# Kernel tuning notes

Measured on AMD Instinct MI355X. Metric: run time of the kernel, lower is better.

Reference implementation:

```python
import jax, jax.numpy as jnp
import numpy as np

B, S, H = 64, 2048, 512
NEG = -1e9

def setup_inputs() -> dict:
    key = jax.random.key(0)
    k1, k2, k3, k4, k5 = jax.random.split(key, 5)
    encoder_outputs = jax.random.normal(k1, (B, S, H), dtype=jnp.float32)
    mask = jax.random.randint(k2, (B, S), 0, 2).astype(bool)
    W = jax.random.normal(k3, (H, H), dtype=jnp.float32) / np.sqrt(H)
    b = jnp.zeros((H,), dtype=jnp.float32)
    v = jax.random.normal(k4, (H,), dtype=jnp.float32)  # context_vector
    return {"encoder_outputs": encoder_outputs, "mask": mask, "W": W, "b": b, "v": v}

def reference(encoder_outputs, mask, W, b, v):
    # u = tanh(x @ W^T + b): [B,S,H]
    u = jnp.tanh(jnp.einsum('bsh,oh->bso', encoder_outputs, W) + b)
    scores = jnp.einsum('bsh,h->bs', u, v)                 # [B,S]
    scores = jnp.where(mask, scores, NEG)
    attn_weights = jax.nn.softmax(scores, axis=1)          # [B,S]
    weighted_output = jnp.einsum('bsh,bs->bh', encoder_outputs, attn_weights)
    return weighted_output, attn_weights
```

## Files before the change

kernel.cpp:

```cpp
#include <hip/hip_runtime.h>
#include <hip/hip_fp16.h>
#include <stdint.h>

#define NEG_ (-1e9f)

typedef _Float16 f16x8 __attribute__((ext_vector_type(8)));
typedef float    f32x4 __attribute__((ext_vector_type(4)));

__device__ __forceinline__ float fast_tanh(float x) {
  float e = __expf(2.0f * x);
  return (e - 1.0f) * __builtin_amdgcn_rcpf(e + 1.0f);
}

__global__ __launch_bounds__(256) void k0_cvt_w(const float* __restrict__ W,
                                                __half* __restrict__ Wws) {
  int g = blockIdx.x * 256 + threadIdx.x;
  int lane = g & 63;
  int seg  = g >> 6;
  int io = seg & 3, ks = (seg >> 2) & 15, w = seg >> 6;
  int o = w * 64 + io * 16 + (lane & 15);
  int k = ks * 32 + (lane >> 4) * 8;
  const float2* src = (const float2*)(W + (size_t)o * 512 + k);
  __half2 h[4];
#pragma unroll
  for (int j = 0; j < 4; ++j) { float2 f = src[j]; h[j] = __floats2half2_rn(f.x, f.y); }
  uint4 u;
  u.x = *(uint32_t*)&h[0]; u.y = *(uint32_t*)&h[1];
  u.z = *(uint32_t*)&h[2]; u.w = *(uint32_t*)&h[3];
  *(uint4*)(Wws + (size_t)seg * 512 + (size_t)lane * 8) = u;
}

__global__ __launch_bounds__(512, 4) void k1_scores(
    const float* __restrict__ enc, const int* __restrict__ msk,
    const float* __restrict__ bias, const float* __restrict__ ctx,
    const __half* __restrict__ Wws, float* __restrict__ scores,
    float* __restrict__ psum, float* __restrict__ mpart,
    float* __restrict__ lpart) {
  __shared__ __align__(16) __half Xl[64 * 512];
  __shared__ float sred[512];
  __shared__ float pbuf[64];

  const int t = threadIdx.x;
  const int w = t >> 6;
  const int lane = t & 63;
  const int quad = lane >> 4;
  const int l15 = lane & 15;
  const size_t mtile = blockIdx.x;

  f16x8 abuf[3][4];
  auto aload = [&](int slot, int ks) {
    const f16x8* sp = (const f16x8*)(Wws +
        ((size_t)(w * 64 + ks * 4) * 512) + (size_t)lane * 8);
#pragma unroll
    for (int io = 0; io < 4; ++io) abuf[slot][io] = sp[io * 64];
  };

  {
    const float4* Xg = (const float4*)(enc + mtile * (size_t)(64 * 512));
    float4 xr[16];
#pragma unroll
    for (int j = 0; j < 8; ++j) {
      int g = j * 512 + t;
      int s = g >> 6, c = g & 63;
      xr[2 * j]     = Xg[s * 128 + 2 * c];
      xr[2 * j + 1] = Xg[s * 128 + 2 * c + 1];
    }
    aload(0, 0);
    aload(1, 1);
#pragma unroll
    for (int j = 0; j < 8; ++j) {
      int g = j * 512 + t;
      int s = g >> 6, c = g & 63;
      float4 x0 = xr[2 * j];
      float4 x1 = xr[2 * j + 1];
      __half2 h0 = __floats2half2_rn(x0.x, x0.y);
      __half2 h1 = __floats2half2_rn(x0.z, x0.w);
      __half2 h2 = __floats2half2_rn(x1.x, x1.y);
      __half2 h3 = __floats2half2_rn(x1.z, x1.w);
      uint4 u;
      u.x = *(uint32_t*)&h0; u.y = *(uint32_t*)&h1;
      u.z = *(uint32_t*)&h2; u.w = *(uint32_t*)&h3;
      int pc = c ^ (s & 7);
      *(uint4*)&Xl[s * 512 + pc * 8] = u;
    }
  }
  __syncthreads();

  f32x4 acc[4][4];
#pragma unroll
  for (int io = 0; io < 4; ++io)
#pragma unroll
    for (int is = 0; is < 4; ++is) acc[io][is] = (f32x4){0.f, 0.f, 0.f, 0.f};

#pragma unroll
  for (int ks = 0; ks < 16; ++ks) {
    if (ks + 2 < 16) aload((ks + 2) % 3, ks + 2);
    const f16x8* acur = abuf[ks % 3];
#pragma unroll
    for (int is = 0; is < 4; ++is) {
      int s = is * 16 + l15;
      const f16x8 bf = *(const f16x8*)&Xl[s * 512 + (((ks * 4 + quad) ^ (s & 7)) << 3)];
#pragma unroll
      for (int io = 0; io < 4; ++io)
        acc[io][is] = __builtin_amdgcn_mfma_f32_16x16x32_f16(acur[io], bf, acc[io][is], 0, 0, 0);
    }
  }

  float ps[4] = {0.f, 0.f, 0.f, 0.f};
#pragma unroll
  for (int io = 0; io < 4; ++io) {
    int ob = w * 64 + io * 16 + quad * 4;
    float4 b4 = *(const float4*)(bias + ob);
    float4 v4 = *(const float4*)(ctx + ob);
#pragma unroll
    for (int is = 0; is < 4; ++is) {
      const f32x4 a = acc[io][is];
      ps[is] += fast_tanh(a[0] + b4.x) * v4.x + fast_tanh(a[1] + b4.y) * v4.y +
                fast_tanh(a[2] + b4.z) * v4.z + fast_tanh(a[3] + b4.w) * v4.w;
    }
  }
#pragma unroll
  for (int is = 0; is < 4; ++is) {
    ps[is] += __shfl_xor(ps[is], 16, 64);
    ps[is] += __shfl_xor(ps[is], 32, 64);
  }

  __syncthreads();
  if (lane < 16) {
#pragma unroll
    for (int is = 0; is < 4; ++is) sred[w * 64 + is * 16 + lane] = ps[is];
  }
  __syncthreads();
  if (t < 64) {
    float sc = 0.f;
#pragma unroll
    for (int k = 0; k < 8; ++k) sc += sred[k * 64 + t];
    size_t row = mtile * 64 + t;
    float sm = msk[row] ? sc : NEG_;
    scores[row] = sm;
    float m = sm;
#pragma unroll
    for (int off = 32; off >= 1; off >>= 1) m = fmaxf(m, __shfl_xor(m, off, 64));
    float p = __expf(sm - m);
    float l = p;
#pragma unroll
    for (int off = 32; off >= 1; off >>= 1) l += __shfl_xor(l, off, 64);
    pbuf[t] = p;
    if (t == 0) { mpart[mtile] = m; lpart[mtile] = l; }
  }
  __syncthreads();

  float pacc[8] = {0.f, 0.f, 0.f, 0.f, 0.f, 0.f, 0.f, 0.f};
  const int c = lane;
#pragma unroll
  for (int si = 0; si < 8; ++si) {
    int s = (w << 3) + si;
    float pv = pbuf[s];
    f16x8 xv = *(const f16x8*)&Xl[s * 512 + ((c ^ (s & 7)) << 3)];
#pragma unroll
    for (int j = 0; j < 8; ++j) pacc[j] = fmaf(pv, (float)xv[j], pacc[j]);
  }
  __syncthreads();
  float* pred = (float*)&Xl[0];
  {
    float4 lo = {pacc[0], pacc[1], pacc[2], pacc[3]};
    float4 hi = {pacc[4], pacc[5], pacc[6], pacc[7]};
    *(float4*)&pred[w * 512 + c * 4] = lo;
    *(float4*)&pred[w * 512 + 256 + c * 4] = hi;
  }
  __syncthreads();
  if (t < 128) {
    int half = t & 1, c2 = t >> 1;
    float4 a = {0.f, 0.f, 0.f, 0.f};
#pragma unroll
    for (int w2 = 0; w2 < 8; ++w2) {
      float4 pv = *(const float4*)&pred[w2 * 512 + half * 256 + c2 * 4];
      a.x += pv.x; a.y += pv.y; a.z += pv.z; a.w += pv.w;
    }
    *(float4*)&psum[mtile * 512 + (size_t)t * 4] = a;
  }
}

__global__ __launch_bounds__(256) void k2_combine(
    float* __restrict__ attn, const float* __restrict__ psum,
    const float* __restrict__ mpart, const float* __restrict__ lpart,
    float* __restrict__ out0) {
  const int b = blockIdx.x >> 3, g = blockIdx.x & 7, t = threadIdx.x;
  __shared__ float ml[32], ll[32];
  if (t < 32) { ml[t] = mpart[b * 32 + t]; ll[t] = lpart[b * 32 + t]; }
  __syncthreads();
  float M = -3.4e38f;
#pragma unroll
  for (int i = 0; i < 32; ++i) M = fmaxf(M, ml[i]);
  float Z = 0.f;
#pragma unroll
  for (int i = 0; i < 32; ++i) Z += __expf(ml[i] - M) * ll[i];
  float invZ = 1.0f / Z;

  {
    int s = g * 256 + t;
    float* row = attn + (size_t)b * 2048;
    row[s] = __expf(row[s] - M) * invZ;
  }

  if (t < 64) {
    int h = g * 64 + t;
    float a = 0.f;
#pragma unroll
    for (int c2 = 0; c2 < 32; ++c2) {
      float wv = __expf(ml[c2] - M);
      a = fmaf(wv, psum[((size_t)(b * 32 + c2)) * 512 + h], a);
    }
    out0[(size_t)b * 512 + h] = a * invZ;
  }
}

extern "C" void kernel_launch(void* const* d_in, const int* in_sizes, int n_in,
                              void* d_out, int out_size, void* d_ws, size_t ws_size,
                              hipStream_t stream) {
  (void)in_sizes; (void)n_in; (void)out_size; (void)ws_size;
  const float* enc  = (const float*)d_in[0];
  const int*   msk  = (const int*)d_in[1];
  const float* W    = (const float*)d_in[2];
  const float* bias = (const float*)d_in[3];
  const float* ctx  = (const float*)d_in[4];
  float* out0 = (float*)d_out;
  float* attn = out0 + 64 * 512;

  __half* Wws  = (__half*)d_ws;
  float*  psum = (float*)((char*)d_ws + (512u << 10));
  float*  mprt = psum + (size_t)2048 * 512;
  float*  lprt = mprt + 2048;

  k0_cvt_w<<<128, 256, 0, stream>>>(W, Wws);
  k1_scores<<<2048, 512, 0, stream>>>(enc, msk, bias, ctx, Wws, attn,
                                      psum, mprt, lprt);
  k2_combine<<<512, 256, 0, stream>>>(attn, psum, mprt, lprt, out0);
}
```

Baseline: 439.8 us.

## Read encoder tile directly from global memory instead of staging it in LDS

Drops the 64KB LDS staging of the fp16-converted encoder tile. Each wave now loads fp32 encoder values straight from global memory inside the MFMA loop, converting them to fp16 in registers, and rereads them from global for the weighted-sum pass. W fragments are loaded per k-step without the triple-buffered prefetch, and the loop is only partially unrolled. This lowers LDS use and may raise occupancy, but each of the 8 waves rereads the same X tile from global or L2, adding memory traffic and exposing load latency to the MFMAs.

```diff
diff --git a/kernel.cpp b/kernel.cpp
--- a/kernel.cpp
+++ b/kernel.cpp
@@ -36,9 +36,9 @@
     const __half* __restrict__ Wws, float* __restrict__ scores,
     float* __restrict__ psum, float* __restrict__ mpart,
     float* __restrict__ lpart) {
-  __shared__ __align__(16) __half Xl[64 * 512];
   __shared__ float sred[512];
   __shared__ float pbuf[64];
+  __shared__ __align__(16) float pred[8 * 512];
 
   const int t = threadIdx.x;
   const int w = t >> 6;
@@ -46,45 +46,7 @@
   const int quad = lane >> 4;
   const int l15 = lane & 15;
   const size_t mtile = blockIdx.x;
-
-  f16x8 abuf[3][4];
-  auto aload = [&](int slot, int ks) {
-    const f16x8* sp = (const f16x8*)(Wws +
-        ((size_t)(w * 64 + ks * 4) * 512) + (size_t)lane * 8);
-#pragma unroll
-    for (int io = 0; io < 4; ++io) abuf[slot][io] = sp[io * 64];
-  };
-
-  {
-    const float4* Xg = (const float4*)(enc + mtile * (size_t)(64 * 512));
-    float4 xr[16];
-#pragma unroll
-    for (int j = 0; j < 8; ++j) {
-      int g = j * 512 + t;
-      int s = g >> 6, c = g & 63;
-      xr[2 * j]     = Xg[s * 128 + 2 * c];
-      xr[2 * j + 1] = Xg[s * 128 + 2 * c + 1];
-    }
-    aload(0, 0);
-    aload(1, 1);
-#pragma unroll
-    for (int j = 0; j < 8; ++j) {
-      int g = j * 512 + t;
-      int s = g >> 6, c = g & 63;
-      float4 x0 = xr[2 * j];
-      float4 x1 = xr[2 * j + 1];
-      __half2 h0 = __floats2half2_rn(x0.x, x0.y);
-      __half2 h1 = __floats2half2_rn(x0.z, x0.w);
-      __half2 h2 = __floats2half2_rn(x1.x, x1.y);
-      __half2 h3 = __floats2half2_rn(x1.z, x1.w);
-      uint4 u;
-      u.x = *(uint32_t*)&h0; u.y = *(uint32_t*)&h1;
-      u.z = *(uint32_t*)&h2; u.w = *(uint32_t*)&h3;
-      int pc = c ^ (s & 7);
-      *(uint4*)&Xl[s * 512 + pc * 8] = u;
-    }
-  }
-  __syncthreads();
+  const float* Xb = enc + mtile * (size_t)(64 * 512);
 
   f32x4 acc[4][4];
 #pragma unroll
@@ -92,17 +54,29 @@
 #pragma unroll
     for (int is = 0; is < 4; ++is) acc[io][is] = (f32x4){0.f, 0.f, 0.f, 0.f};
 
-#pragma unroll
+#pragma unroll 2
   for (int ks = 0; ks < 16; ++ks) {
-    if (ks + 2 < 16) aload((ks + 2) % 3, ks + 2);
-    const f16x8* acur = abuf[ks % 3];
+    f16x8 af[4];
+    {
+      const f16x8* sp = (const f16x8*)(Wws +
+          ((size_t)(w * 64 + ks * 4) * 512) + (size_t)lane * 8);
+#pragma unroll
+      for (int io = 0; io < 4; ++io) af[io] = sp[io * 64];
+    }
 #pragma unroll
     for (int is = 0; is < 4; ++is) {
       int s = is * 16 + l15;
-      const f16x8 bf = *(const f16x8*)&Xl[s * 512 + (((ks * 4 + quad) ^ (s & 7)) << 3)];
+      const float* bp = Xb + (size_t)s * 512 + ks * 32 + quad * 8;
+      f32x4 xa = *(const f32x4*)bp;
+      f32x4 xb = *(const f32x4*)(bp + 4);
+      f16x8 bf;
+      bf[0] = (_Float16)xa[0]; bf[1] = (_Float16)xa[1];
+      bf[2] = (_Float16)xa[2]; bf[3] = (_Float16)xa[3];
+      bf[4] = (_Float16)xb[0]; bf[5] = (_Float16)xb[1];
+      bf[6] = (_Float16)xb[2]; bf[7] = (_Float16)xb[3];
 #pragma unroll
       for (int io = 0; io < 4; ++io)
-        acc[io][is] = __builtin_amdgcn_mfma_f32_16x16x32_f16(acur[io], bf, acc[io][is], 0, 0, 0);
+        acc[io][is] = __builtin_amdgcn_mfma_f32_16x16x32_f16(af[io], bf, acc[io][is], 0, 0, 0);
     }
   }
 
@@ -125,7 +99,6 @@
     ps[is] += __shfl_xor(ps[is], 32, 64);
   }
 
-  __syncthreads();
   if (lane < 16) {
 #pragma unroll
     for (int is = 0; is < 4; ++is) sred[w * 64 + is * 16 + lane] = ps[is];
@@ -151,22 +124,27 @@
   __syncthreads();
 
   float pacc[8] = {0.f, 0.f, 0.f, 0.f, 0.f, 0.f, 0.f, 0.f};
-  const int c = lane;
 #pragma unroll
   for (int si = 0; si < 8; ++si) {
     int s = (w << 3) + si;
     float pv = pbuf[s];
-    f16x8 xv = *(const f16x8*)&Xl[s * 512 + ((c ^ (s & 7)) << 3)];
-#pragma unroll
-    for (int j = 0; j < 8; ++j) pacc[j] = fmaf(pv, (float)xv[j], pacc[j]);
-  }
-  __syncthreads();
-  float* pred = (float*)&Xl[0];
+    const float* xp = Xb + (size_t)s * 512 + lane * 8;
+    f32x4 xa = *(const f32x4*)xp;
+    f32x4 xb = *(const f32x4*)(xp + 4);
+    pacc[0] = fmaf(pv, xa[0], pacc[0]);
+    pacc[1] = fmaf(pv, xa[1], pacc[1]);
+    pacc[2] = fmaf(pv, xa[2], pacc[2]);
+    pacc[3] = fmaf(pv, xa[3], pacc[3]);
+    pacc[4] = fmaf(pv, xb[0], pacc[4]);
+    pacc[5] = fmaf(pv, xb[1], pacc[5]);
+    pacc[6] = fmaf(pv, xb[2], pacc[6]);
+    pacc[7] = fmaf(pv, xb[3], pacc[7]);
+  }
   {
     float4 lo = {pacc[0], pacc[1], pacc[2], pacc[3]};
     float4 hi = {pacc[4], pacc[5], pacc[6], pacc[7]};
-    *(float4*)&pred[w * 512 + c * 4] = lo;
-    *(float4*)&pred[w * 512 + 256 + c * 4] = hi;
+    *(float4*)&pred[w * 512 + lane * 4] = lo;
+    *(float4*)&pred[w * 512 + 256 + lane * 4] = hi;
   }
   __syncthreads();
   if (t < 128) {
```

Result: slower. 596.3 us (+35.6%).
